# Kernel optimization log

Measured on AMD Instinct MI355X. Metric: run time of the kernel, lower is better.

Reference implementation:

```python
import jax, jax.numpy as jnp
import numpy as np

B, T, F_IN, D_PROJ, D_M, NH, DH, D_FF, OUT = 512, 100, 384, 128, 100, 4, 25, 400, 100
KS, SIGMA = 5, 1.0

def gaussian_kernel(size, sigma):
    c = jnp.arange(size, dtype=jnp.float32) - (size - 1) / 2.0
    x, y = jnp.meshgrid(c, c, indexing='ij')  # torch.meshgrid default is 'ij'
    k = jnp.exp(-(x ** 2 + y ** 2) / (2.0 * sigma ** 2))
    return k / k.sum()

def layer_norm(x, g, b, eps=1e-5):
    m = x.mean(-1, keepdims=True)
    v = ((x - m) ** 2).mean(-1, keepdims=True)
    return (x - m) / jnp.sqrt(v + eps) * g + b

def setup_inputs():
    key = jax.random.key(0)
    ks = jax.random.split(key, 20)
    la = jax.random.randint(ks[0], (B,), 2, T + 1)
    lc = jax.random.randint(ks[1], (B,), 2, T + 1)
    ar = jnp.arange(T)
    anchor_mask = (ar[None, :] < la[:, None]).astype(jnp.float32)
    comparison_mask = (ar[None, :] < lc[:, None]).astype(jnp.float32)
    p = lambda k, sh: jax.random.normal(k, sh, jnp.float32) * 0.02
    return dict(
        anco_speech=jax.random.normal(ks[2], (B, T, F_IN), jnp.float32),
        anchor_mask=anchor_mask,
        com_speech=jax.random.normal(ks[3], (B, T, F_IN), jnp.float32),
        comparison_mask=comparison_mask,
        anco_text=jax.random.normal(ks[4], (B, 128, 768), jnp.float32),
        label=jax.random.uniform(ks[5], (B,), jnp.float32),
        ln_an_g=jnp.ones(F_IN), ln_an_b=jnp.zeros(F_IN),
        W_an=p(ks[6], (F_IN, D_PROJ)), b_an=jnp.zeros(D_PROJ),
        ln_com_g=jnp.ones(F_IN), ln_com_b=jnp.zeros(F_IN),
        W_com=p(ks[7], (F_IN, D_PROJ)), b_com=jnp.zeros(D_PROJ),
        Wq=p(ks[8], (D_M, D_M)), bq=jnp.zeros(D_M),
        Wk=p(ks[9], (D_M, D_M)), bk=jnp.zeros(D_M),
        Wv=p(ks[10], (D_M, D_M)), bv=jnp.zeros(D_M),
        Wo=p(ks[11], (D_M, D_M)), bo=jnp.zeros(D_M),
        ln1_g=jnp.ones(D_M), ln1_b=jnp.zeros(D_M),
        Wff1=p(ks[12], (D_M, D_FF)), bff1=jnp.zeros(D_FF),
        Wff2=p(ks[13], (D_FF, D_M)), bff2=jnp.zeros(D_M),
        ln2_g=jnp.ones(D_M), ln2_b=jnp.zeros(D_M),
        W_ih=p(ks[14], (3 * OUT, D_M)), W_hh=p(ks[15], (3 * OUT, OUT)),
        b_ih=jnp.zeros(3 * OUT), b_hh=jnp.zeros(3 * OUT),
        W_fc=p(ks[16], (OUT, OUT)), b_fc=jnp.zeros(OUT),
        W_dense=p(ks[17], (OUT, 1)), b_dense=jnp.zeros(1))

def _bilinear_to_TxT(s, na, nc):
    # align_corners=True bilinear upsample of the valid [na, nc] top-left block of s to [T, T]
    t = jnp.arange(T, dtype=jnp.float32)
    sr = t * (na - 1).astype(jnp.float32) / (T - 1)
    sc = t * (nc - 1).astype(jnp.float32) / (T - 1)
    r0 = jnp.floor(sr).astype(jnp.int32); r1 = jnp.minimum(r0 + 1, na - 1); wr = sr - r0
    c0 = jnp.floor(sc).astype(jnp.int32); c1 = jnp.minimum(c0 + 1, nc - 1); wc = sc - c0
    v00 = s[r0[:, None], c0[None, :]]; v01 = s[r0[:, None], c1[None, :]]
    v10 = s[r1[:, None], c0[None, :]]; v11 = s[r1[:, None], c1[None, :]]
    top = v00 * (1 - wc)[None, :] + v01 * wc[None, :]
    bot = v10 * (1 - wc)[None, :] + v11 * wc[None, :]
    return top * (1 - wr)[:, None] + bot * wr[:, None]

def _forward(anco_speech, anchor_mask, com_speech, comparison_mask,
             ln_an_g, ln_an_b, W_an, b_an, ln_com_g, ln_com_b, W_com, b_com,
             Wq, bq, Wk, bk, Wv, bv, Wo, bo, ln1_g, ln1_b, Wff1, bff1, Wff2, bff2,
             ln2_g, ln2_b, W_ih, W_hh, b_ih, b_hh, W_fc, b_fc, W_dense, b_dense):
    # Projection adapters (LayerNorm -> Linear -> SiLU)
    an_p = jax.nn.silu(layer_norm(anco_speech, ln_an_g, ln_an_b) @ W_an + b_an)
    co_p = jax.nn.silu(layer_norm(com_speech, ln_com_g, ln_com_b) @ W_com + b_com)
    # masked cross cosine similarity [B, T, T]
    an_n = an_p / jnp.clip(jnp.linalg.norm(an_p, axis=-1, keepdims=True), 1e-8)
    co_n = co_p / jnp.clip(jnp.linalg.norm(co_p, axis=-1, keepdims=True), 1e-8)
    sim = jnp.einsum('bid,bjd->bij', an_n, co_n)
    sim = sim * anchor_mask[:, :, None] * comparison_mask[:, None, :]
    # ragged per-sample bilinear upsample of valid block to (100,100), vectorized via vmap
    la = anchor_mask.sum(1).astype(jnp.int32)
    lc = comparison_mask.sum(1).astype(jnp.int32)
    up = jax.vmap(_bilinear_to_TxT)(sim, la, lc)  # [B, T, T]
    # gaussian smoothing, kernel 5, padding 2 (== SAME)
    gk = gaussian_kernel(KS, SIGMA)[None, None]  # [1,1,5,5]
    sm = jax.lax.conv_general_dilated(up[:, None], gk, (1, 1), 'SAME',
                                      dimension_numbers=('NCHW', 'OIHW', 'NCHW'))[:, 0]
    # transformer encoder layer (post-norm, relu, 4 heads)
    q = (sm @ Wq + bq).reshape(B, T, NH, DH)
    k = (sm @ Wk + bk).reshape(B, T, NH, DH)
    v = (sm @ Wv + bv).reshape(B, T, NH, DH)
    att = jax.nn.softmax(jnp.einsum('bihd,bjhd->bhij', q, k) / np.float32(np.sqrt(DH)), axis=-1)
    ao = jnp.einsum('bhij,bjhd->bihd', att, v).reshape(B, T, D_M) @ Wo + bo
    x = layer_norm(sm + ao, ln1_g, ln1_b)
    x = layer_norm(x + jax.nn.relu(x @ Wff1 + bff1) @ Wff2 + bff2, ln2_g, ln2_b)
    # GRU over time, keep last hidden
    def step(h, xt):
        gi = xt @ W_ih.T + b_ih
        gh = h @ W_hh.T + b_hh
        ir, iz, inn = jnp.split(gi, 3, -1)
        hr, hz, hn = jnp.split(gh, 3, -1)
        r = jax.nn.sigmoid(ir + hr)
        z = jax.nn.sigmoid(iz + hz)
        n = jnp.tanh(inn + r * hn)
        return (1 - z) * n + z * h, None
    h0 = jnp.zeros((B, OUT), x.dtype)
    hT, _ = jax.lax.scan(step, h0, x.transpose(1, 0, 2))
    return (hT @ W_fc + b_fc) @ W_dense + b_dense  # [B, 1]

def reference(anco_speech, anchor_mask, com_speech, comparison_mask, anco_text, label,
              ln_an_g, ln_an_b, W_an, b_an, ln_com_g, ln_com_b, W_com, b_com,
              Wq, bq, Wk, bk, Wv, bv, Wo, bo, ln1_g, ln1_b, Wff1, bff1, Wff2, bff2,
              ln2_g, ln2_b, W_ih, W_hh, b_ih, b_hh, W_fc, b_fc, W_dense, b_dense):
    # anco_text and label are unused by the original forward
    return _forward(anco_speech, anchor_mask, com_speech, comparison_mask,
                    ln_an_g, ln_an_b, W_an, b_an, ln_com_g, ln_com_b, W_com, b_com,
                    Wq, bq, Wk, bk, Wv, bv, Wo, bo, ln1_g, ln1_b, Wff1, bff1, Wff2, bff2,
                    ln2_g, ln2_b, W_ih, W_hh, b_ih, b_hh, W_fc, b_fc, W_dense, b_dense)
```

## Files before the change

kernel.cpp:

```cpp
#include <hip/hip_runtime.h>
#include <cmath>

#define NB 512
#define NT 100
#define NROW (NB*NT)
#define FIN 384
#define DP 128

struct GW { float w[5]; };

__global__ __launch_bounds__(128) void k_lalc(const float* __restrict__ am, const float* __restrict__ cm,
                                              int* __restrict__ la, int* __restrict__ lc)
{
  __shared__ float s0[128], s1[128];
  int b = blockIdx.x, tid = threadIdx.x;
  s0[tid] = (tid < NT) ? am[b*NT+tid] : 0.0f;
  s1[tid] = (tid < NT) ? cm[b*NT+tid] : 0.0f;
  __syncthreads();
  for (int off = 64; off > 0; off >>= 1) {
    if (tid < off) { s0[tid] += s0[tid+off]; s1[tid] += s1[tid+off]; }
    __syncthreads();
  }
  if (tid == 0) { la[b] = (int)(s0[0] + 0.5f); lc[b] = (int)(s1[0] + 0.5f); }
}

__global__ __launch_bounds__(256) void k1_proj(
    const float* __restrict__ xin, const float* __restrict__ lng, const float* __restrict__ lnb,
    const float* __restrict__ W, const float* __restrict__ bias, float* __restrict__ out)
{
  const int tid = threadIdx.x;
  const int row0 = blockIdx.x * 32;
  __shared__ float xs[32*388];
  __shared__ float ps[256];
  __shared__ float ms[32];
  __shared__ float rs[32];
  __shared__ float inorm[32];

  const float4* x4 = (const float4*)(xin + (size_t)row0*FIN);
  for (int idx = tid; idx < 32*96; idx += 256) {
    int r = idx/96, k4 = idx%96;
    ((float4*)xs)[r*97 + k4] = x4[idx];
  }
  __syncthreads();
  {
    int r = tid>>3, p = tid&7;
    float s = 0; const float* xr = xs + r*388 + p*48;
    #pragma unroll
    for (int k=0;k<48;k++) s += xr[k];
    ps[tid] = s;
  }
  __syncthreads();
  if (tid < 32) { float s=0; for (int p=0;p<8;p++) s += ps[tid*8+p]; ms[tid] = s*(1.0f/FIN); }
  __syncthreads();
  {
    int r = tid>>3, p = tid&7;
    float m = ms[r], s=0; const float* xr = xs + r*388 + p*48;
    for (int k=0;k<48;k++){ float d = xr[k]-m; s += d*d; }
    ps[tid] = s;
  }
  __syncthreads();
  if (tid < 32) { float s=0; for (int p=0;p<8;p++) s += ps[tid*8+p]; rs[tid] = rsqrtf(s*(1.0f/FIN) + 1e-5f); }
  __syncthreads();
  for (int idx = tid; idx < 32*FIN; idx += 256) {
    int r = idx/FIN, k = idx%FIN;
    xs[r*388+k] = (xs[r*388+k]-ms[r])*rs[r]*lng[k] + lnb[k];
  }
  __syncthreads();
  const int jg = tid & 31, rg = tid >> 5;
  float acc[4][4] = {};
  const float4* W4 = (const float4*)W;
  for (int k = 0; k < FIN; k++) {
    float4 wv = W4[k*32 + jg];
    #pragma unroll
    for (int rr = 0; rr < 4; rr++) {
      float xv = xs[(rg*4+rr)*388 + k];
      acc[rr][0] += xv*wv.x; acc[rr][1] += xv*wv.y;
      acc[rr][2] += xv*wv.z; acc[rr][3] += xv*wv.w;
    }
  }
  __syncthreads();
  #pragma unroll
  for (int rr = 0; rr < 4; rr++) {
    int r = rg*4+rr;
    #pragma unroll
    for (int c = 0; c < 4; c++) {
      float pv = acc[rr][c] + bias[jg*4+c];
      xs[r*132 + jg*4 + c] = pv * (1.0f/(1.0f+__expf(-pv)));
    }
  }
  __syncthreads();
  {
    int r = tid>>3, p = tid&7;
    float s = 0; const float* xr = xs + r*132 + p*16;
    #pragma unroll
    for (int k=0;k<16;k++) s += xr[k]*xr[k];
    ps[tid] = s;
  }
  __syncthreads();
  if (tid < 32) { float s=0; for (int p=0;p<8;p++) s += ps[tid*8+p]; inorm[tid] = 1.0f/fmaxf(sqrtf(s), 1e-8f); }
  __syncthreads();
  float4* o4 = (float4*)(out + (size_t)row0*DP);
  for (int idx = tid; idx < 32*32; idx += 256) {
    int r = idx/32, k4 = idx%32;
    float4 v = ((float4*)xs)[r*33 + k4];
    float s = inorm[r];
    v.x*=s; v.y*=s; v.z*=s; v.w*=s;
    o4[idx] = v;
  }
}

__global__ __launch_bounds__(256) void k2_sim(const float* __restrict__ An, const float* __restrict__ Co,
                                              float* __restrict__ S)
{
  int b = blockIdx.x, tid = threadIdx.x;
  __shared__ float as_[100*132];
  __shared__ float bs_[100*132];
  const float4* A4 = (const float4*)(An + (size_t)b*NT*DP);
  const float4* B4 = (const float4*)(Co + (size_t)b*NT*DP);
  for (int idx = tid; idx < 100*32; idx += 256) {
    int r = idx>>5, k4 = idx&31;
    ((float4*)as_)[r*33+k4] = A4[idx];
    ((float4*)bs_)[r*33+k4] = B4[idx];
  }
  __syncthreads();
  int ti = tid>>4, tj = tid&15;
  float acc[7][7] = {};
  for (int k4 = 0; k4 < 32; k4++) {
    float4 av[7], bv[7];
    #pragma unroll
    for (int m=0;m<7;m++){ int i = ti+16*m; if (i>99) i=99; av[m] = ((float4*)as_)[i*33+k4]; }
    #pragma unroll
    for (int n=0;n<7;n++){ int j = tj+16*n; if (j>99) j=99; bv[n] = ((float4*)bs_)[j*33+k4]; }
    #pragma unroll
    for (int m=0;m<7;m++)
      #pragma unroll
      for (int n=0;n<7;n++)
        acc[m][n] += av[m].x*bv[n].x + av[m].y*bv[n].y + av[m].z*bv[n].z + av[m].w*bv[n].w;
  }
  float* Sb = S + (size_t)b*NT*NT;
  #pragma unroll
  for (int m=0;m<7;m++){ int i = ti+16*m; if (i>99) continue;
    #pragma unroll
    for (int n=0;n<7;n++){ int j = tj+16*n; if (j>99) continue;
      Sb[i*100+j] = acc[m][n];
    } }
}

__global__ __launch_bounds__(256) void k3_bilinear(const float* __restrict__ S, float* __restrict__ U,
                                                   const int* __restrict__ la, const int* __restrict__ lc)
{
  int b = blockIdx.x, tid = threadIdx.x;
  int na = la[b], nc = lc[b];
  const float* Sb = S + (size_t)b*10000;
  float* Ub = U + (size_t)b*10000;
  for (int idx = tid; idx < 10000; idx += 256) {
    int i = idx/100, j = idx%100;
    float sr = (float)(i*(na-1)) / 99.0f;
    float sc = (float)(j*(nc-1)) / 99.0f;
    int r0 = (int)sr, c0 = (int)sc;
    float wr = sr - (float)r0, wc = sc - (float)c0;
    int r1 = r0+1; if (r1 > na-1) r1 = na-1;
    int c1 = c0+1; if (c1 > nc-1) c1 = nc-1;
    float v00 = Sb[r0*100+c0], v01 = Sb[r0*100+c1];
    float v10 = Sb[r1*100+c0], v11 = Sb[r1*100+c1];
    float top = v00*(1.0f-wc) + v01*wc;
    float bot = v10*(1.0f-wc) + v11*wc;
    Ub[idx] = top*(1.0f-wr) + bot*wr;
  }
}

__global__ __launch_bounds__(256) void k4_conv(const float* __restrict__ U, float* __restrict__ S, GW gw)
{
  int b = blockIdx.x, tid = threadIdx.x;
  __shared__ float us[100*104];
  __shared__ float ts[100*104];
  const float4* U4 = (const float4*)(U + (size_t)b*10000);
  for (int idx = tid; idx < 100*25; idx += 256) {
    int r = idx/25, k4 = idx%25;
    ((float4*)us)[r*26+k4] = U4[idx];
  }
  __syncthreads();
  for (int idx = tid; idx < 10000; idx += 256) {
    int i = idx/100, j = idx%100;
    float s = 0;
    #pragma unroll
    for (int d = -2; d <= 2; d++) {
      int jj = j + d;
      if (jj >= 0 && jj < 100) s += gw.w[d+2] * us[i*104+jj];
    }
    ts[i*104+j] = s;
  }
  __syncthreads();
  float* Sb = S + (size_t)b*10000;
  for (int idx = tid; idx < 10000; idx += 256) {
    int i = idx/100, j = idx%100;
    float s = 0;
    #pragma unroll
    for (int d = -2; d <= 2; d++) {
      int ii = i + d;
      if (ii >= 0 && ii < 100) s += gw.w[d+2] * ts[ii*104+j];
    }
    Sb[idx] = s;
  }
}

__global__ __launch_bounds__(256) void k5_qkv(const float* __restrict__ SM,
    const float* __restrict__ Wq, const float* __restrict__ bq,
    const float* __restrict__ Wk, const float* __restrict__ bk,
    const float* __restrict__ Wv, const float* __restrict__ bv,
    float* __restrict__ Q, float* __restrict__ K, float* __restrict__ V)
{
  int tid = threadIdx.x;
  int row0 = blockIdx.x * 32;
  __shared__ float xs[32*104];
  const float4* X4 = (const float4*)(SM + (size_t)row0*100);
  for (int idx = tid; idx < 32*25; idx += 256) {
    int r = idx/25, k4 = idx%25;
    ((float4*)xs)[r*26+k4] = X4[idx];
  }
  __syncthreads();
  int jg = tid&31, rg = tid>>5;
  for (int jt = 0; jt < 3; jt++) {
    int j0 = jt*128 + jg*4;
    if (j0 < 300) {
      const float* Wsel; const float* bsel; float* Osel; int jj;
      if (j0 < 100)      { Wsel=Wq; bsel=bq; Osel=Q; jj=j0; }
      else if (j0 < 200) { Wsel=Wk; bsel=bk; Osel=K; jj=j0-100; }
      else               { Wsel=Wv; bsel=bv; Osel=V; jj=j0-200; }
      float acc[4][4] = {};
      const float4* W4 = (const float4*)Wsel;
      for (int k = 0; k < 100; k++) {
        float4 wv = W4[k*25 + (jj>>2)];
        #pragma unroll
        for (int rr=0; rr<4; rr++) {
          float xv = xs[(rg*4+rr)*104 + k];
          acc[rr][0]+=xv*wv.x; acc[rr][1]+=xv*wv.y; acc[rr][2]+=xv*wv.z; acc[rr][3]+=xv*wv.w;
        }
      }
      float4 bv4 = ((const float4*)bsel)[jj>>2];
      #pragma unroll
      for (int rr=0; rr<4; rr++) {
        int r = row0 + rg*4 + rr;
        float4 o; o.x=acc[rr][0]+bv4.x; o.y=acc[rr][1]+bv4.y; o.z=acc[rr][2]+bv4.z; o.w=acc[rr][3]+bv4.w;
        *(float4*)(Osel + (size_t)r*100 + jj) = o;
      }
    }
  }
}

__global__ __launch_bounds__(256) void k6_attn(const float* __restrict__ Q, const float* __restrict__ K,
                                               const float* __restrict__ V, float* __restrict__ HO)
{
  int b = blockIdx.x, h = blockIdx.y, tid = threadIdx.x;
  __shared__ float qs[100*28], ks[100*28], vs[100*28];
  __shared__ float ss[100*101];
  for (int idx = tid; idx < 2500; idx += 256) {
    int r = idx/25, d = idx%25;
    size_t g = (size_t)(b*100+r)*100 + h*25 + d;
    qs[r*28+d] = Q[g]; ks[r*28+d] = K[g]; vs[r*28+d] = V[g];
  }
  __syncthreads();
  int ti = tid>>4, tj = tid&15;
  {
    float acc[7][7] = {};
    for (int d4 = 0; d4 < 6; d4++) {
      float4 qv[7], kv[7];
      #pragma unroll
      for (int m=0;m<7;m++){ int i=ti+16*m; if(i>99)i=99; qv[m]=((float4*)qs)[i*7+d4]; }
      #pragma unroll
      for (int n=0;n<7;n++){ int j=tj+16*n; if(j>99)j=99; kv[n]=((float4*)ks)[j*7+d4]; }
      #pragma unroll
      for (int m=0;m<7;m++)
        #pragma unroll
        for (int n=0;n<7;n++)
          acc[m][n] += qv[m].x*kv[n].x + qv[m].y*kv[n].y + qv[m].z*kv[n].z + qv[m].w*kv[n].w;
    }
    {
      float qv[7], kv[7];
      #pragma unroll
      for (int m=0;m<7;m++){ int i=ti+16*m; if(i>99)i=99; qv[m]=qs[i*28+24]; }
      #pragma unroll
      for (int n=0;n<7;n++){ int j=tj+16*n; if(j>99)j=99; kv[n]=ks[j*28+24]; }
      #pragma unroll
      for (int m=0;m<7;m++)
        #pragma unroll
        for (int n=0;n<7;n++) acc[m][n] += qv[m]*kv[n];
    }
    #pragma unroll
    for (int m=0;m<7;m++){ int i=ti+16*m; if (i>99) continue;
      #pragma unroll
      for (int n=0;n<7;n++){ int j=tj+16*n; if (j>99) continue;
        ss[i*101+j] = acc[m][n]*(1.0f/5.0f);
      } }
  }
  __syncthreads();
  if (tid < 100) {
    float* row = ss + tid*101;
    float mx = -1e30f;
    for (int j=0;j<100;j++) mx = fmaxf(mx, row[j]);
    float sum = 0;
    for (int j=0;j<100;j++){ float e = __expf(row[j]-mx); row[j] = e; sum += e; }
    float inv = 1.0f/sum;
    for (int j=0;j<100;j++) row[j] *= inv;
  }
  __syncthreads();
  {
    int d0 = tj;
    float acc0[7] = {}, acc1[7] = {};
    for (int j = 0; j < 100; j++) {
      float v0 = vs[j*28 + d0];
      float v1 = (tj < 9) ? vs[j*28 + d0 + 16] : 0.0f;
      #pragma unroll
      for (int m=0;m<7;m++) {
        int i = ti+16*m; if (i>99) i = 99;
        float p = ss[i*101+j];
        acc0[m] += p*v0; acc1[m] += p*v1;
      }
    }
    #pragma unroll
    for (int m=0;m<7;m++) {
      int i = ti+16*m; if (i>99) continue;
      size_t g = (size_t)(b*100+i)*100 + h*25;
      HO[g + d0] = acc0[m];
      if (tj < 9) HO[g + d0 + 16] = acc1[m];
    }
  }
}

__device__ __forceinline__ void row_ln_100(float* ybuf, float* ps, float* ms, float* rs,
                                           const float* g, const float* bta, int tid)
{
  {
    int r = tid>>3, p = tid&7;
    int kb = p*13, ke = kb+13; if (ke>100) ke=100;
    float s=0; const float* yr = ybuf + r*104;
    for (int k=kb;k<ke;k++) s += yr[k];
    ps[tid]=s;
  }
  __syncthreads();
  if (tid<32){ float s=0; for(int p=0;p<8;p++) s+=ps[tid*8+p]; ms[tid]=s*(1.0f/100.0f); }
  __syncthreads();
  {
    int r = tid>>3, p = tid&7;
    int kb = p*13, ke = kb+13; if (ke>100) ke=100;
    float m = ms[r], s=0; const float* yr = ybuf + r*104;
    for (int k=kb;k<ke;k++){ float d=yr[k]-m; s+=d*d; }
    ps[tid]=s;
  }
  __syncthreads();
  if (tid<32){ float s=0; for(int p=0;p<8;p++) s+=ps[tid*8+p]; rs[tid]=rsqrtf(s*(1.0f/100.0f)+1e-5f); }
  __syncthreads();
  for (int idx=tid; idx<3200; idx+=256){
    int r = idx/100, k = idx%100;
    ybuf[r*104+k] = (ybuf[r*104+k]-ms[r])*rs[r]*g[k] + bta[k];
  }
  __syncthreads();
}

__global__ __launch_bounds__(256) void k7_ln1(const float* __restrict__ HOin, const float* __restrict__ Wo,
    const float* __restrict__ bo, const float* __restrict__ SM,
    const float* __restrict__ g1, const float* __restrict__ b1v, float* __restrict__ X)
{
  int tid = threadIdx.x;
  int row0 = blockIdx.x * 32;
  __shared__ float hsd[32*104];
  __shared__ float ys[32*104];
  __shared__ float ps[256];
  __shared__ float ms[32], rs[32];
  const float4* H4 = (const float4*)(HOin + (size_t)row0*100);
  for (int idx = tid; idx < 32*25; idx += 256) {
    int r = idx/25, k4 = idx%25;
    ((float4*)hsd)[r*26+k4] = H4[idx];
  }
  __syncthreads();
  int jg = tid&31, rg = tid>>5;
  if (jg < 25) {
    int j0 = jg*4;
    float acc[4][4] = {};
    const float4* W4 = (const float4*)Wo;
    for (int k=0;k<100;k++) {
      float4 wv = W4[k*25 + jg];
      #pragma unroll
      for (int rr=0;rr<4;rr++){
        float xv = hsd[(rg*4+rr)*104+k];
        acc[rr][0]+=xv*wv.x; acc[rr][1]+=xv*wv.y; acc[rr][2]+=xv*wv.z; acc[rr][3]+=xv*wv.w;
      }
    }
    float4 bv = ((const float4*)bo)[jg];
    #pragma unroll
    for (int rr=0;rr<4;rr++){
      int r = rg*4+rr;
      float4 smv = ((const float4*)(SM + (size_t)(row0+r)*100))[jg];
      float4 o; o.x = acc[rr][0]+bv.x+smv.x; o.y = acc[rr][1]+bv.y+smv.y;
      o.z = acc[rr][2]+bv.z+smv.z; o.w = acc[rr][3]+bv.w+smv.w;
      *(float4*)&ys[r*104 + j0] = o;
    }
  }
  __syncthreads();
  row_ln_100(ys, ps, ms, rs, g1, b1v, tid);
  float4* X4o = (float4*)(X + (size_t)row0*100);
  for (int idx=tid; idx<32*25; idx+=256){
    int r = idx/25, k4 = idx%25;
    X4o[idx] = ((float4*)ys)[r*26+k4];
  }
}

__global__ __launch_bounds__(256) void k8_ffn(const float* __restrict__ X,
    const float* __restrict__ W1, const float* __restrict__ b1f,
    const float* __restrict__ W2, const float* __restrict__ b2f,
    const float* __restrict__ g2, const float* __restrict__ bt2, float* __restrict__ X2)
{
  int tid = threadIdx.x;
  int row0 = blockIdx.x * 32;
  __shared__ float xs[32*104];
  __shared__ float hh[32*404];
  __shared__ float ps[256];
  __shared__ float ms[32], rs[32];
  const float4* X4 = (const float4*)(X + (size_t)row0*100);
  for (int idx = tid; idx < 32*25; idx += 256) {
    int r=idx/25,k4=idx%25; ((float4*)xs)[r*26+k4] = X4[idx];
  }
  __syncthreads();
  int jg = tid&31, rg = tid>>5;
  const float4* W14 = (const float4*)W1;
  for (int jt = 0; jt < 4; jt++) {
    int j0 = jt*128 + jg*4;
    if (j0 < 400) {
      float acc[4][4] = {};
      for (int k=0;k<100;k++){
        float4 wv = W14[k*100 + (j0>>2)];
        #pragma unroll
        for (int rr=0;rr<4;rr++){
          float xv = xs[(rg*4+rr)*104+k];
          acc[rr][0]+=xv*wv.x; acc[rr][1]+=xv*wv.y; acc[rr][2]+=xv*wv.z; acc[rr][3]+=xv*wv.w;
        }
      }
      float4 bv = ((const float4*)b1f)[j0>>2];
      #pragma unroll
      for (int rr=0;rr<4;rr++){
        int r = rg*4+rr;
        float4 o;
        o.x=fmaxf(acc[rr][0]+bv.x,0.0f); o.y=fmaxf(acc[rr][1]+bv.y,0.0f);
        o.z=fmaxf(acc[rr][2]+bv.z,0.0f); o.w=fmaxf(acc[rr][3]+bv.w,0.0f);
        *(float4*)&hh[r*404 + j0] = o;
      }
    }
  }
  __syncthreads();
  float4 yv[4];
  if (jg < 25) {
    int j0 = jg*4;
    float acc[4][4] = {};
    const float4* W24 = (const float4*)W2;
    for (int k=0;k<400;k++){
      float4 wv = W24[k*25 + jg];
      #pragma unroll
      for (int rr=0;rr<4;rr++){
        float xv = hh[(rg*4+rr)*404+k];
        acc[rr][0]+=xv*wv.x; acc[rr][1]+=xv*wv.y; acc[rr][2]+=xv*wv.z; acc[rr][3]+=xv*wv.w;
      }
    }
    float4 bv = ((const float4*)b2f)[jg];
    #pragma unroll
    for (int rr=0;rr<4;rr++){
      int r=rg*4+rr;
      yv[rr].x=acc[rr][0]+bv.x+xs[r*104+j0+0];
      yv[rr].y=acc[rr][1]+bv.y+xs[r*104+j0+1];
      yv[rr].z=acc[rr][2]+bv.z+xs[r*104+j0+2];
      yv[rr].w=acc[rr][3]+bv.w+xs[r*104+j0+3];
    }
  }
  __syncthreads();
  if (jg < 25) {
    int j0 = jg*4;
    #pragma unroll
    for (int rr=0;rr<4;rr++) *(float4*)&xs[(rg*4+rr)*104+j0] = yv[rr];
  }
  __syncthreads();
  row_ln_100(xs, ps, ms, rs, g2, bt2, tid);
  float4* O4 = (float4*)(X2 + (size_t)row0*100);
  for (int idx=tid; idx<32*25; idx+=256){
    int r=idx/25,k4=idx%25; O4[idx] = ((float4*)xs)[r*26+k4];
  }
}

__global__ void k_tr(const float* __restrict__ A, float* __restrict__ AT)
{
  int idx = blockIdx.x*256 + threadIdx.x;
  if (idx < 300*100){ int g = idx/100, k = idx%100; AT[k*300+g] = A[idx]; }
}

__global__ __launch_bounds__(256) void k9_gi(const float* __restrict__ X2, const float* __restrict__ WT,
    const float* __restrict__ bih, float* __restrict__ GIv)
{
  int tid = threadIdx.x;
  int row0 = blockIdx.x * 32;
  __shared__ float xs[32*104];
  const float4* X4 = (const float4*)(X2 + (size_t)row0*100);
  for (int idx = tid; idx < 32*25; idx += 256){ int r=idx/25,k4=idx%25; ((float4*)xs)[r*26+k4]=X4[idx]; }
  __syncthreads();
  int jg = tid&31, rg = tid>>5;
  const float4* W4 = (const float4*)WT;
  for (int jt=0; jt<3; jt++){
    int j0 = jt*128 + jg*4;
    if (j0 < 300) {
      float acc[4][4] = {};
      for (int k=0;k<100;k++){
        float4 wv = W4[k*75 + (j0>>2)];
        #pragma unroll
        for (int rr=0;rr<4;rr++){
          float xv = xs[(rg*4+rr)*104+k];
          acc[rr][0]+=xv*wv.x; acc[rr][1]+=xv*wv.y; acc[rr][2]+=xv*wv.z; acc[rr][3]+=xv*wv.w;
        }
      }
      float4 bv = ((const float4*)bih)[j0>>2];
      #pragma unroll
      for (int rr=0;rr<4;rr++){
        int r = row0 + rg*4+rr;
        int bb = r/100, t = r%100;
        float4 o; o.x=acc[rr][0]+bv.x; o.y=acc[rr][1]+bv.y; o.z=acc[rr][2]+bv.z; o.w=acc[rr][3]+bv.w;
        *(float4*)(GIv + ((size_t)t*512 + bb)*300 + j0) = o;
      }
    }
  }
}

__global__ __launch_bounds__(320) void k10_gru(const float* __restrict__ GIv, const float* __restrict__ Whh,
    const float* __restrict__ bhh, float* __restrict__ HT)
{
  int tid = threadIdx.x;
  int r0 = blockIdx.x*2;
  __shared__ float4 W4[7500];
  __shared__ float hs[2][100];
  __shared__ float ghs[2][300];
  __shared__ float gis[2][300];
  __shared__ float bhs[300];
  const float4* Wg4 = (const float4*)Whh;
  for (int idx = tid; idx < 7500; idx += 320) {
    int g = idx/25, k4 = idx%25;
    W4[k4*300+g] = Wg4[g*25+k4];
  }
  if (tid < 300) bhs[tid] = bhh[tid];
  if (tid < 200) hs[tid/100][tid%100] = 0.0f;
  __syncthreads();
  for (int t = 0; t < 100; t++) {
    if (tid < 300) {
      gis[0][tid] = GIv[((size_t)t*512 + r0)*300 + tid];
      gis[1][tid] = GIv[((size_t)t*512 + r0+1)*300 + tid];
      float a0 = 0, a1 = 0;
      const float4* h40 = (const float4*)hs[0];
      const float4* h41 = (const float4*)hs[1];
      #pragma unroll
      for (int k4 = 0; k4 < 25; k4++) {
        float4 w = W4[k4*300 + tid];
        float4 h0 = h40[k4];
        float4 h1 = h41[k4];
        a0 += w.x*h0.x + w.y*h0.y + w.z*h0.z + w.w*h0.w;
        a1 += w.x*h1.x + w.y*h1.y + w.z*h1.z + w.w*h1.w;
      }
      float bb = bhs[tid];
      ghs[0][tid] = a0 + bb;
      ghs[1][tid] = a1 + bb;
    }
    __syncthreads();
    if (tid < 200) {
      int rr = tid/100, j = tid%100;
      float rg = 1.0f/(1.0f+__expf(-(gis[rr][j]     + ghs[rr][j])));
      float zg = 1.0f/(1.0f+__expf(-(gis[rr][j+100] + ghs[rr][j+100])));
      float ng = tanhf(gis[rr][j+200] + rg*ghs[rr][j+200]);
      float hold = hs[rr][j];
      hs[rr][j] = (1.0f-zg)*ng + zg*hold;
    }
    __syncthreads();
  }
  if (tid < 200) HT[(size_t)(r0 + tid/100)*100 + tid%100] = hs[tid/100][tid%100];
}

__global__ __launch_bounds__(128) void k_out(const float* __restrict__ HT, const float* __restrict__ Wfc,
    const float* __restrict__ bfc, const float* __restrict__ Wd, const float* __restrict__ bd,
    float* __restrict__ out)
{
  __shared__ float red[128];
  int b = blockIdx.x, tid = threadIdx.x;
  float s = 0;
  if (tid < 100) {
    float v = 0;
    for (int j = 0; j < 100; j++) v += Wfc[tid*100+j]*Wd[j];
    s = HT[(size_t)b*100+tid]*v + bfc[tid]*Wd[tid];
  }
  red[tid] = s;
  __syncthreads();
  for (int off = 64; off > 0; off >>= 1) {
    if (tid < off) red[tid] += red[tid+off];
    __syncthreads();
  }
  if (tid == 0) out[b] = red[0] + bd[0];
}

extern "C" void kernel_launch(void* const* d_in, const int* in_sizes, int n_in,
                              void* d_out, int out_size, void* d_ws, size_t ws_size,
                              hipStream_t stream)
{
  const float* anco  = (const float*)d_in[0];
  const float* amask = (const float*)d_in[1];
  const float* comsp = (const float*)d_in[2];
  const float* cmask = (const float*)d_in[3];
  const float* ln_an_g = (const float*)d_in[6];
  const float* ln_an_b = (const float*)d_in[7];
  const float* W_an  = (const float*)d_in[8];
  const float* b_an  = (const float*)d_in[9];
  const float* ln_co_g = (const float*)d_in[10];
  const float* ln_co_b = (const float*)d_in[11];
  const float* W_co  = (const float*)d_in[12];
  const float* b_co  = (const float*)d_in[13];
  const float* Wq = (const float*)d_in[14]; const float* bq = (const float*)d_in[15];
  const float* Wk = (const float*)d_in[16]; const float* bk = (const float*)d_in[17];
  const float* Wv = (const float*)d_in[18]; const float* bv = (const float*)d_in[19];
  const float* Wo = (const float*)d_in[20]; const float* bo = (const float*)d_in[21];
  const float* ln1g = (const float*)d_in[22]; const float* ln1b = (const float*)d_in[23];
  const float* W1 = (const float*)d_in[24]; const float* b1 = (const float*)d_in[25];
  const float* W2 = (const float*)d_in[26]; const float* b2 = (const float*)d_in[27];
  const float* ln2g = (const float*)d_in[28]; const float* ln2b = (const float*)d_in[29];
  const float* Wih = (const float*)d_in[30]; const float* Whh = (const float*)d_in[31];
  const float* bih = (const float*)d_in[32]; const float* bhh = (const float*)d_in[33];
  const float* Wfc = (const float*)d_in[34]; const float* bfc = (const float*)d_in[35];
  const float* Wd  = (const float*)d_in[36]; const float* bd  = (const float*)d_in[37];

  float* ws = (float*)d_ws;
  float* AN = ws;
  float* CO = ws + 6553600;
  float* S  = ws + 13107200;
  float* U  = ws + 18227200;
  float* Dh = ws + 23347200;
  float* GIp = ws + 13107200;
  float* HT = ws + 28467200;
  float* WT = ws + 28518400;
  int* la = (int*)(ws + 28548500);
  int* lc = la + 512;

  GW gw;
  {
    float e[5], sum = 0;
    for (int i=0;i<5;i++){ float c = (float)i - 2.0f; e[i] = expf(-(c*c)/2.0f); sum += e[i]; }
    for (int i=0;i<5;i++) gw.w[i] = e[i]/sum;
  }

  k_lalc<<<512,128,0,stream>>>(amask, cmask, la, lc);
  k1_proj<<<1600,256,0,stream>>>(anco,  ln_an_g, ln_an_b, W_an, b_an, AN);
  k1_proj<<<1600,256,0,stream>>>(comsp, ln_co_g, ln_co_b, W_co, b_co, CO);
  k2_sim<<<512,256,0,stream>>>(AN, CO, S);
  k3_bilinear<<<512,256,0,stream>>>(S, U, la, lc);
  k4_conv<<<512,256,0,stream>>>(U, S, gw);
  k5_qkv<<<1600,256,0,stream>>>(S, Wq,bq, Wk,bk, Wv,bv, AN, CO, U);
  k6_attn<<<dim3(512,4),256,0,stream>>>(AN, CO, U, Dh);
  k7_ln1<<<1600,256,0,stream>>>(Dh, Wo, bo, S, ln1g, ln1b, AN);
  k8_ffn<<<1600,256,0,stream>>>(AN, W1,b1, W2,b2, ln2g, ln2b, CO);
  k_tr<<<118,256,0,stream>>>(Wih, WT);
  k9_gi<<<1600,256,0,stream>>>(CO, WT, bih, GIp);
  k10_gru<<<256,320,0,stream>>>(GIp, Whh, bhh, HT);
  k_out<<<512,128,0,stream>>>(HT, Wfc, bfc, Wd, bd, (float*)d_out);
}
```

Measured before the change: 1.461 ms.

## Port projection, QKV, FFN and GRU-input GEMMs to bf16 MFMA

Adds a prep kernel that transposes and pads the weights into bf16. The input projection, QKV, FFN and GRU input-gate matmuls now run on bf16 16x16x32 MFMA instructions instead of scalar fp32 FMA loops. The FFN's LayerNorm is redone with wave shuffles, and its output is stored as padded bf16 that feeds k9 directly, which also removes the separate Wih transpose kernel. Rounding activations and weights to bf16 lowers precision, and there is one extra prep launch per call.

```diff
diff --git a/kernel.cpp b/kernel.cpp
--- a/kernel.cpp
+++ b/kernel.cpp
@@ -9,6 +9,44 @@
 
 struct GW { float w[5]; };
 
+typedef __attribute__((ext_vector_type(8))) short bf16x8;
+typedef __attribute__((ext_vector_type(4))) float f32x4;
+
+__device__ __forceinline__ unsigned short f2bf(float f){
+  union { float f; unsigned u; } v; v.f = f;
+  unsigned u = v.u;
+  return (unsigned short)((u + 0x7FFFu + ((u>>16)&1u)) >> 16);
+}
+__device__ __forceinline__ float bf2f(unsigned short h){
+  union { unsigned u; float f; } v; v.u = ((unsigned)h)<<16; return v.f;
+}
+
+__global__ __launch_bounds__(256) void k_prep(const float* __restrict__ Wan, const float* __restrict__ Wco,
+    const float* __restrict__ Wq, const float* __restrict__ Wk, const float* __restrict__ Wv,
+    const float* __restrict__ bq, const float* __restrict__ bk, const float* __restrict__ bv,
+    const float* __restrict__ W1, const float* __restrict__ W2, const float* __restrict__ Wih,
+    unsigned short* __restrict__ WanT, unsigned short* __restrict__ WcoT,
+    unsigned short* __restrict__ WqkvT, unsigned short* __restrict__ W1T,
+    unsigned short* __restrict__ W2T, unsigned short* __restrict__ WihT,
+    float* __restrict__ bqkv)
+{
+  int idx = blockIdx.x*256 + threadIdx.x;
+  if (idx < 49152) { int j = idx/384, k = idx%384; WanT[idx] = f2bf(Wan[k*128+j]); }
+  else if (idx < 98304) { int i = idx-49152; int j = i/384, k = i%384; WcoT[i] = f2bf(Wco[k*128+j]); }
+  else if (idx < 137216) { int i = idx-98304; int j = i/128, k = i%128;
+    float v = 0.0f;
+    if (k < 100 && j < 300) v = (j < 100) ? Wq[k*100+j] : ((j < 200) ? Wk[k*100+j-100] : Wv[k*100+j-200]);
+    WqkvT[i] = f2bf(v); }
+  else if (idx < 188416) { int i = idx-137216; int j = i/128, k = i%128;
+    W1T[i] = f2bf(k < 100 ? W1[k*400+j] : 0.0f); }
+  else if (idx < 238592) { int i = idx-188416; int j = i/448, k = i%448;
+    W2T[i] = f2bf((j < 100 && k < 400) ? W2[k*100+j] : 0.0f); }
+  else if (idx < 277504) { int i = idx-238592; int j = i/128, k = i%128;
+    WihT[i] = f2bf((k < 100 && j < 300) ? Wih[j*100+k] : 0.0f); }
+  else if (idx < 277804) { int j = idx-277504;
+    bqkv[j] = (j < 100) ? bq[j] : ((j < 200) ? bk[j-100] : bv[j-200]); }
+}
+
 __global__ __launch_bounds__(128) void k_lalc(const float* __restrict__ am, const float* __restrict__ cm,
                                               int* __restrict__ la, int* __restrict__ lc)
 {
@@ -26,25 +64,24 @@
 
 __global__ __launch_bounds__(256) void k1_proj(
     const float* __restrict__ xin, const float* __restrict__ lng, const float* __restrict__ lnb,
-    const float* __restrict__ W, const float* __restrict__ bias, float* __restrict__ out)
+    const unsigned short* __restrict__ WT, const float* __restrict__ bias, float* __restrict__ out)
 {
   const int tid = threadIdx.x;
   const int row0 = blockIdx.x * 32;
-  __shared__ float xs[32*388];
+  __shared__ float xf[32*388];
   __shared__ float ps[256];
-  __shared__ float ms[32];
-  __shared__ float rs[32];
-  __shared__ float inorm[32];
+  __shared__ float ms[32], rs[32], inorm[32];
+  float* ys = xf;
 
   const float4* x4 = (const float4*)(xin + (size_t)row0*FIN);
   for (int idx = tid; idx < 32*96; idx += 256) {
     int r = idx/96, k4 = idx%96;
-    ((float4*)xs)[r*97 + k4] = x4[idx];
+    ((float4*)xf)[r*97 + k4] = x4[idx];
   }
   __syncthreads();
   {
     int r = tid>>3, p = tid&7;
-    float s = 0; const float* xr = xs + r*388 + p*48;
+    float s = 0; const float* xr = xf + r*388 + p*48;
     #pragma unroll
     for (int k=0;k<48;k++) s += xr[k];
     ps[tid] = s;
@@ -54,7 +91,7 @@
   __syncthreads();
   {
     int r = tid>>3, p = tid&7;
-    float m = ms[r], s=0; const float* xr = xs + r*388 + p*48;
+    float m = ms[r], s=0; const float* xr = xf + r*388 + p*48;
     for (int k=0;k<48;k++){ float d = xr[k]-m; s += d*d; }
     ps[tid] = s;
   }
@@ -63,35 +100,49 @@
   __syncthreads();
   for (int idx = tid; idx < 32*FIN; idx += 256) {
     int r = idx/FIN, k = idx%FIN;
-    xs[r*388+k] = (xs[r*388+k]-ms[r])*rs[r]*lng[k] + lnb[k];
-  }
-  __syncthreads();
-  const int jg = tid & 31, rg = tid >> 5;
-  float acc[4][4] = {};
-  const float4* W4 = (const float4*)W;
-  for (int k = 0; k < FIN; k++) {
-    float4 wv = W4[k*32 + jg];
-    #pragma unroll
-    for (int rr = 0; rr < 4; rr++) {
-      float xv = xs[(rg*4+rr)*388 + k];
-      acc[rr][0] += xv*wv.x; acc[rr][1] += xv*wv.y;
-      acc[rr][2] += xv*wv.z; acc[rr][3] += xv*wv.w;
-    }
-  }
-  __syncthreads();
-  #pragma unroll
-  for (int rr = 0; rr < 4; rr++) {
-    int r = rg*4+rr;
-    #pragma unroll
-    for (int c = 0; c < 4; c++) {
-      float pv = acc[rr][c] + bias[jg*4+c];
-      xs[r*132 + jg*4 + c] = pv * (1.0f/(1.0f+__expf(-pv)));
+    xf[r*388+k] = (xf[r*388+k]-ms[r])*rs[r]*lng[k] + lnb[k];
+  }
+  __syncthreads();
+  const int l = tid & 63, w = tid >> 6;
+  const int lh = l & 15, lq = l >> 4;
+  const int rt = w & 1, nh = w >> 1;
+  bf16x8 afr[12];
+  {
+    const int row = rt*16 + lh;
+    const float* xr = &xf[row*388 + lq*8];
+    #pragma unroll
+    for (int kb = 0; kb < 12; kb++) {
+      float4 u0 = *(const float4*)(xr + kb*32);
+      float4 u1 = *(const float4*)(xr + kb*32 + 4);
+      bf16x8 a;
+      a[0]=(short)f2bf(u0.x); a[1]=(short)f2bf(u0.y); a[2]=(short)f2bf(u0.z); a[3]=(short)f2bf(u0.w);
+      a[4]=(short)f2bf(u1.x); a[5]=(short)f2bf(u1.y); a[6]=(short)f2bf(u1.z); a[7]=(short)f2bf(u1.w);
+      afr[kb] = a;
+    }
+  }
+  __syncthreads();
+  for (int nt2 = 0; nt2 < 4; nt2++) {
+    int nt = nh*4 + nt2;
+    int j = nt*16 + lh;
+    f32x4 acc = {0.f,0.f,0.f,0.f};
+    const unsigned short* wp = &WT[(size_t)j*384 + lq*8];
+    #pragma unroll
+    for (int kb = 0; kb < 12; kb++) {
+      bf16x8 b = *(const bf16x8*)(wp + kb*32);
+      acc = __builtin_amdgcn_mfma_f32_16x16x32_bf16(afr[kb], b, acc, 0, 0, 0);
+    }
+    float bj = bias[j];
+    #pragma unroll
+    for (int p = 0; p < 4; p++) {
+      float v = acc[p] + bj;
+      v = v * (1.0f/(1.0f+__expf(-v)));
+      ys[(rt*16 + lq*4 + p)*132 + j] = v;
     }
   }
   __syncthreads();
   {
     int r = tid>>3, p = tid&7;
-    float s = 0; const float* xr = xs + r*132 + p*16;
+    float s = 0; const float* xr = ys + r*132 + p*16;
     #pragma unroll
     for (int k=0;k<16;k++) s += xr[k]*xr[k];
     ps[tid] = s;
@@ -102,7 +153,7 @@
   float4* o4 = (float4*)(out + (size_t)row0*DP);
   for (int idx = tid; idx < 32*32; idx += 256) {
     int r = idx/32, k4 = idx%32;
-    float4 v = ((float4*)xs)[r*33 + k4];
+    float4 v = ((float4*)ys)[r*33 + k4];
     float s = inorm[r];
     v.x*=s; v.y*=s; v.z*=s; v.w*=s;
     o4[idx] = v;
@@ -205,45 +256,51 @@
 }
 
 __global__ __launch_bounds__(256) void k5_qkv(const float* __restrict__ SM,
-    const float* __restrict__ Wq, const float* __restrict__ bq,
-    const float* __restrict__ Wk, const float* __restrict__ bk,
-    const float* __restrict__ Wv, const float* __restrict__ bv,
+    const unsigned short* __restrict__ WT, const float* __restrict__ bqkv,
     float* __restrict__ Q, float* __restrict__ K, float* __restrict__ V)
 {
-  int tid = threadIdx.x;
-  int row0 = blockIdx.x * 32;
-  __shared__ float xs[32*104];
+  const int tid = threadIdx.x;
+  const int row0 = blockIdx.x * 64;
+  __shared__ unsigned short xsb[64*128];
   const float4* X4 = (const float4*)(SM + (size_t)row0*100);
-  for (int idx = tid; idx < 32*25; idx += 256) {
+  for (int idx = tid; idx < 64*25; idx += 256) {
     int r = idx/25, k4 = idx%25;
-    ((float4*)xs)[r*26+k4] = X4[idx];
-  }
-  __syncthreads();
-  int jg = tid&31, rg = tid>>5;
-  for (int jt = 0; jt < 3; jt++) {
-    int j0 = jt*128 + jg*4;
-    if (j0 < 300) {
-      const float* Wsel; const float* bsel; float* Osel; int jj;
-      if (j0 < 100)      { Wsel=Wq; bsel=bq; Osel=Q; jj=j0; }
-      else if (j0 < 200) { Wsel=Wk; bsel=bk; Osel=K; jj=j0-100; }
-      else               { Wsel=Wv; bsel=bv; Osel=V; jj=j0-200; }
-      float acc[4][4] = {};
-      const float4* W4 = (const float4*)Wsel;
-      for (int k = 0; k < 100; k++) {
-        float4 wv = W4[k*25 + (jj>>2)];
-        #pragma unroll
-        for (int rr=0; rr<4; rr++) {
-          float xv = xs[(rg*4+rr)*104 + k];
-          acc[rr][0]+=xv*wv.x; acc[rr][1]+=xv*wv.y; acc[rr][2]+=xv*wv.z; acc[rr][3]+=xv*wv.w;
-        }
-      }
-      float4 bv4 = ((const float4*)bsel)[jj>>2];
-      #pragma unroll
-      for (int rr=0; rr<4; rr++) {
-        int r = row0 + rg*4 + rr;
-        float4 o; o.x=acc[rr][0]+bv4.x; o.y=acc[rr][1]+bv4.y; o.z=acc[rr][2]+bv4.z; o.w=acc[rr][3]+bv4.w;
-        *(float4*)(Osel + (size_t)r*100 + jj) = o;
-      }
+    float4 v = X4[idx];
+    ushort4 pk = make_ushort4(f2bf(v.x), f2bf(v.y), f2bf(v.z), f2bf(v.w));
+    *(ushort4*)&xsb[r*128 + ((k4*4) ^ ((r&7)<<3))] = pk;
+  }
+  for (int idx = tid; idx < 64*28; idx += 256) {
+    int r = idx/28, k = 100 + idx%28;
+    xsb[r*128 + (k ^ ((r&7)<<3))] = 0;
+  }
+  __syncthreads();
+  const int l = tid & 63, w = tid >> 6;
+  const int lh = l & 15, lq = l >> 4;
+  const int arow = w*16 + lh;
+  bf16x8 afr[4];
+  #pragma unroll
+  for (int kb = 0; kb < 4; kb++)
+    afr[kb] = *(const bf16x8*)&xsb[arow*128 + ((kb*32 + lq*8) ^ ((arow&7)<<3))];
+  int orow[4];
+  #pragma unroll
+  for (int p=0;p<4;p++) orow[p] = row0 + w*16 + lq*4 + p;
+  for (int nt = 0; nt < 19; nt++) {
+    int j = nt*16 + lh;
+    f32x4 acc = {0.f,0.f,0.f,0.f};
+    const unsigned short* wp = &WT[(size_t)j*128 + lq*8];
+    #pragma unroll
+    for (int kb = 0; kb < 4; kb++) {
+      bf16x8 b = *(const bf16x8*)(wp + kb*32);
+      acc = __builtin_amdgcn_mfma_f32_16x16x32_bf16(afr[kb], b, acc, 0, 0, 0);
+    }
+    if (j < 300) {
+      float bj = bqkv[j];
+      float* dst; int col;
+      if (j < 100)      { dst = Q; col = j; }
+      else if (j < 200) { dst = K; col = j-100; }
+      else              { dst = V; col = j-200; }
+      #pragma unroll
+      for (int p=0;p<4;p++) dst[(size_t)orow[p]*100 + col] = acc[p] + bj;
     }
   }
 }
@@ -406,121 +463,156 @@
 }
 
 __global__ __launch_bounds__(256) void k8_ffn(const float* __restrict__ X,
-    const float* __restrict__ W1, const float* __restrict__ b1f,
-    const float* __restrict__ W2, const float* __restrict__ b2f,
-    const float* __restrict__ g2, const float* __restrict__ bt2, float* __restrict__ X2)
-{
-  int tid = threadIdx.x;
-  int row0 = blockIdx.x * 32;
-  __shared__ float xs[32*104];
-  __shared__ float hh[32*404];
-  __shared__ float ps[256];
-  __shared__ float ms[32], rs[32];
+    const unsigned short* __restrict__ W1T, const float* __restrict__ b1f,
+    const unsigned short* __restrict__ W2T, const float* __restrict__ b2f,
+    const float* __restrict__ g2, const float* __restrict__ bt2,
+    unsigned short* __restrict__ X2bf)
+{
+  const int tid = threadIdx.x;
+  const int row0 = blockIdx.x * 64;
+  __shared__ unsigned short xsb[64*128];
+  __shared__ unsigned short hh[64*448];
   const float4* X4 = (const float4*)(X + (size_t)row0*100);
-  for (int idx = tid; idx < 32*25; idx += 256) {
-    int r=idx/25,k4=idx%25; ((float4*)xs)[r*26+k4] = X4[idx];
-  }
-  __syncthreads();
-  int jg = tid&31, rg = tid>>5;
-  const float4* W14 = (const float4*)W1;
-  for (int jt = 0; jt < 4; jt++) {
-    int j0 = jt*128 + jg*4;
-    if (j0 < 400) {
-      float acc[4][4] = {};
-      for (int k=0;k<100;k++){
-        float4 wv = W14[k*100 + (j0>>2)];
-        #pragma unroll
-        for (int rr=0;rr<4;rr++){
-          float xv = xs[(rg*4+rr)*104+k];
-          acc[rr][0]+=xv*wv.x; acc[rr][1]+=xv*wv.y; acc[rr][2]+=xv*wv.z; acc[rr][3]+=xv*wv.w;
-        }
-      }
-      float4 bv = ((const float4*)b1f)[j0>>2];
-      #pragma unroll
-      for (int rr=0;rr<4;rr++){
-        int r = rg*4+rr;
-        float4 o;
-        o.x=fmaxf(acc[rr][0]+bv.x,0.0f); o.y=fmaxf(acc[rr][1]+bv.y,0.0f);
-        o.z=fmaxf(acc[rr][2]+bv.z,0.0f); o.w=fmaxf(acc[rr][3]+bv.w,0.0f);
-        *(float4*)&hh[r*404 + j0] = o;
-      }
-    }
-  }
-  __syncthreads();
-  float4 yv[4];
-  if (jg < 25) {
-    int j0 = jg*4;
-    float acc[4][4] = {};
-    const float4* W24 = (const float4*)W2;
-    for (int k=0;k<400;k++){
-      float4 wv = W24[k*25 + jg];
-      #pragma unroll
-      for (int rr=0;rr<4;rr++){
-        float xv = hh[(rg*4+rr)*404+k];
-        acc[rr][0]+=xv*wv.x; acc[rr][1]+=xv*wv.y; acc[rr][2]+=xv*wv.z; acc[rr][3]+=xv*wv.w;
-      }
-    }
-    float4 bv = ((const float4*)b2f)[jg];
-    #pragma unroll
-    for (int rr=0;rr<4;rr++){
-      int r=rg*4+rr;
-      yv[rr].x=acc[rr][0]+bv.x+xs[r*104+j0+0];
-      yv[rr].y=acc[rr][1]+bv.y+xs[r*104+j0+1];
-      yv[rr].z=acc[rr][2]+bv.z+xs[r*104+j0+2];
-      yv[rr].w=acc[rr][3]+bv.w+xs[r*104+j0+3];
-    }
-  }
-  __syncthreads();
-  if (jg < 25) {
-    int j0 = jg*4;
-    #pragma unroll
-    for (int rr=0;rr<4;rr++) *(float4*)&xs[(rg*4+rr)*104+j0] = yv[rr];
-  }
-  __syncthreads();
-  row_ln_100(xs, ps, ms, rs, g2, bt2, tid);
-  float4* O4 = (float4*)(X2 + (size_t)row0*100);
-  for (int idx=tid; idx<32*25; idx+=256){
-    int r=idx/25,k4=idx%25; O4[idx] = ((float4*)xs)[r*26+k4];
-  }
-}
-
-__global__ void k_tr(const float* __restrict__ A, float* __restrict__ AT)
-{
-  int idx = blockIdx.x*256 + threadIdx.x;
-  if (idx < 300*100){ int g = idx/100, k = idx%100; AT[k*300+g] = A[idx]; }
-}
-
-__global__ __launch_bounds__(256) void k9_gi(const float* __restrict__ X2, const float* __restrict__ WT,
-    const float* __restrict__ bih, float* __restrict__ GIv)
-{
-  int tid = threadIdx.x;
-  int row0 = blockIdx.x * 32;
-  __shared__ float xs[32*104];
-  const float4* X4 = (const float4*)(X2 + (size_t)row0*100);
-  for (int idx = tid; idx < 32*25; idx += 256){ int r=idx/25,k4=idx%25; ((float4*)xs)[r*26+k4]=X4[idx]; }
-  __syncthreads();
-  int jg = tid&31, rg = tid>>5;
-  const float4* W4 = (const float4*)WT;
-  for (int jt=0; jt<3; jt++){
-    int j0 = jt*128 + jg*4;
-    if (j0 < 300) {
-      float acc[4][4] = {};
-      for (int k=0;k<100;k++){
-        float4 wv = W4[k*75 + (j0>>2)];
-        #pragma unroll
-        for (int rr=0;rr<4;rr++){
-          float xv = xs[(rg*4+rr)*104+k];
-          acc[rr][0]+=xv*wv.x; acc[rr][1]+=xv*wv.y; acc[rr][2]+=xv*wv.z; acc[rr][3]+=xv*wv.w;
-        }
-      }
-      float4 bv = ((const float4*)bih)[j0>>2];
-      #pragma unroll
-      for (int rr=0;rr<4;rr++){
-        int r = row0 + rg*4+rr;
-        int bb = r/100, t = r%100;
-        float4 o; o.x=acc[rr][0]+bv.x; o.y=acc[rr][1]+bv.y; o.z=acc[rr][2]+bv.z; o.w=acc[rr][3]+bv.w;
-        *(float4*)(GIv + ((size_t)t*512 + bb)*300 + j0) = o;
-      }
+  for (int idx = tid; idx < 64*25; idx += 256) {
+    int r = idx/25, k4 = idx%25;
+    float4 v = X4[idx];
+    ushort4 pk = make_ushort4(f2bf(v.x), f2bf(v.y), f2bf(v.z), f2bf(v.w));
+    *(ushort4*)&xsb[r*128 + ((k4*4) ^ ((r&7)<<3))] = pk;
+  }
+  for (int idx = tid; idx < 64*28; idx += 256) {
+    int r = idx/28, k = 100 + idx%28;
+    xsb[r*128 + (k ^ ((r&7)<<3))] = 0;
+  }
+  __syncthreads();
+  const int l = tid & 63, w = tid >> 6;
+  const int lh = l & 15, lq = l >> 4;
+  const int arow = w*16 + lh;
+  bf16x8 a1[4];
+  #pragma unroll
+  for (int kb=0;kb<4;kb++)
+    a1[kb] = *(const bf16x8*)&xsb[arow*128 + ((kb*32+lq*8) ^ ((arow&7)<<3))];
+  int drow[4];
+  #pragma unroll
+  for (int p=0;p<4;p++) drow[p] = w*16 + lq*4 + p;
+  for (int nt = 0; nt < 25; nt++) {
+    int j = nt*16 + lh;
+    f32x4 acc = {0.f,0.f,0.f,0.f};
+    const unsigned short* wp = &W1T[(size_t)j*128 + lq*8];
+    #pragma unroll
+    for (int kb=0;kb<4;kb++) {
+      bf16x8 b = *(const bf16x8*)(wp + kb*32);
+      acc = __builtin_amdgcn_mfma_f32_16x16x32_bf16(a1[kb], b, acc, 0, 0, 0);
+    }
+    float bj = b1f[j];
+    #pragma unroll
+    for (int p=0;p<4;p++) {
+      float hv = fmaxf(acc[p] + bj, 0.0f);
+      hh[drow[p]*448 + (j ^ ((drow[p]&7)<<3))] = f2bf(hv);
+    }
+  }
+  for (int i = l; i < 16*48; i += 64) {
+    int r = w*16 + i/48, c = 400 + i%48;
+    hh[r*448 + (c ^ ((r&7)<<3))] = 0;
+  }
+  bf16x8 a2[13];
+  #pragma unroll
+  for (int kb=0;kb<13;kb++)
+    a2[kb] = *(const bf16x8*)&hh[arow*448 + ((kb*32+lq*8) ^ ((arow&7)<<3))];
+  __syncthreads();
+  unsigned short* ob = hh;
+  float y[7][4];
+  #pragma unroll
+  for (int nt=0; nt<7; nt++) {
+    int j = nt*16 + lh;
+    f32x4 acc = {0.f,0.f,0.f,0.f};
+    const unsigned short* wp = &W2T[(size_t)j*448 + lq*8];
+    #pragma unroll
+    for (int kb=0;kb<13;kb++) {
+      bf16x8 b = *(const bf16x8*)(wp + kb*32);
+      acc = __builtin_amdgcn_mfma_f32_16x16x32_bf16(a2[kb], b, acc, 0, 0, 0);
+    }
+    bool valid = (j < 100);
+    float bj = valid ? b2f[j] : 0.0f;
+    #pragma unroll
+    for (int p=0;p<4;p++) {
+      float resid = valid ? bf2f(xsb[drow[p]*128 + (j ^ ((drow[p]&7)<<3))]) : 0.0f;
+      y[nt][p] = valid ? (acc[p] + bj + resid) : 0.0f;
+    }
+  }
+  float mm[4], ri[4];
+  #pragma unroll
+  for (int p=0;p<4;p++) {
+    float s = 0;
+    #pragma unroll
+    for (int nt=0;nt<7;nt++) s += y[nt][p];
+    s += __shfl_xor(s,1); s += __shfl_xor(s,2); s += __shfl_xor(s,4); s += __shfl_xor(s,8);
+    mm[p] = s * 0.01f;
+    float v = 0;
+    #pragma unroll
+    for (int nt=0;nt<7;nt++) {
+      int j = nt*16+lh;
+      if (j < 100) { float d = y[nt][p]-mm[p]; v += d*d; }
+    }
+    v += __shfl_xor(v,1); v += __shfl_xor(v,2); v += __shfl_xor(v,4); v += __shfl_xor(v,8);
+    ri[p] = rsqrtf(v*0.01f + 1e-5f);
+  }
+  #pragma unroll
+  for (int nt=0;nt<7;nt++) {
+    int j = nt*16+lh;
+    float gj = (j<100) ? g2[j] : 0.0f;
+    float bj = (j<100) ? bt2[j] : 0.0f;
+    #pragma unroll
+    for (int p=0;p<4;p++) {
+      unsigned short o = 0;
+      if (j < 100) o = f2bf((y[nt][p]-mm[p])*ri[p]*gj + bj);
+      ob[drow[p]*128 + (j ^ ((drow[p]&7)<<3))] = o;
+    }
+  }
+  #pragma unroll
+  for (int p=0;p<4;p++) {
+    int c = 112 + lh;
+    ob[drow[p]*128 + (c ^ ((drow[p]&7)<<3))] = 0;
+  }
+  __syncthreads();
+  ushort4* dst4 = (ushort4*)(X2bf + (size_t)row0*128);
+  for (int idx = tid; idx < 64*32; idx += 256) {
+    int r = idx/32, c4 = idx%32;
+    dst4[idx] = *(const ushort4*)&ob[r*128 + ((c4*4) ^ ((r&7)<<3))];
+  }
+}
+
+__global__ __launch_bounds__(256) void k9_gi(const unsigned short* __restrict__ X2bf,
+    const unsigned short* __restrict__ WihT, const float* __restrict__ bih, float* __restrict__ GIv)
+{
+  const int tid = threadIdx.x;
+  const int row0 = blockIdx.x * 64;
+  const int l = tid & 63, w = tid >> 6;
+  const int lh = l & 15, lq = l >> 4;
+  const int row = row0 + w*16 + lh;
+  bf16x8 afr[4];
+  #pragma unroll
+  for (int kb=0;kb<4;kb++)
+    afr[kb] = *(const bf16x8*)&X2bf[(size_t)row*128 + kb*32 + lq*8];
+  size_t obase[4];
+  #pragma unroll
+  for (int p=0;p<4;p++) {
+    int gr = row0 + w*16 + lq*4 + p;
+    int bb = gr/100, t = gr%100;
+    obase[p] = ((size_t)t*512 + bb)*300;
+  }
+  for (int nt=0; nt<19; nt++) {
+    int j = nt*16 + lh;
+    f32x4 acc = {0.f,0.f,0.f,0.f};
+    const unsigned short* wp = &WihT[(size_t)j*128 + lq*8];
+    #pragma unroll
+    for (int kb=0;kb<4;kb++) {
+      bf16x8 b = *(const bf16x8*)(wp + kb*32);
+      acc = __builtin_amdgcn_mfma_f32_16x16x32_bf16(afr[kb], b, acc, 0, 0, 0);
+    }
+    if (j < 300) {
+      float bj = bih[j];
+      #pragma unroll
+      for (int p=0;p<4;p++) GIv[obase[p] + j] = acc[p] + bj;
     }
   }
 }
@@ -634,9 +726,17 @@
   float* Dh = ws + 23347200;
   float* GIp = ws + 13107200;
   float* HT = ws + 28467200;
-  float* WT = ws + 28518400;
-  int* la = (int*)(ws + 28548500);
+  int* la = (int*)(ws + 28518400);
   int* lc = la + 512;
+  unsigned short* X2bf = (unsigned short*)CO;
+  unsigned short* WB = (unsigned short*)(ws + 28520000);
+  unsigned short* WanT  = WB;
+  unsigned short* WcoT  = WB + 49152;
+  unsigned short* WqkvT = WB + 98304;
+  unsigned short* W1T   = WB + 137216;
+  unsigned short* W2T   = WB + 188416;
+  unsigned short* WihT  = WB + 238592;
+  float* bqkv = ws + 28660000;
 
   GW gw;
   {
@@ -645,18 +745,19 @@
     for (int i=0;i<5;i++) gw.w[i] = e[i]/sum;
   }
 
+  k_prep<<<1086,256,0,stream>>>(W_an, W_co, Wq, Wk, Wv, bq, bk, bv, W1, W2, Wih,
+                                WanT, WcoT, WqkvT, W1T, W2T, WihT, bqkv);
   k_lalc<<<512,128,0,stream>>>(amask, cmask, la, lc);
-  k1_proj<<<1600,256,0,stream>>>(anco,  ln_an_g, ln_an_b, W_an, b_an, AN);
-  k1_proj<<<1600,256,0,stream>>>(comsp, ln_co_g, ln_co_b, W_co, b_co, CO);
+  k1_proj<<<1600,256,0,stream>>>(anco,  ln_an_g, ln_an_b, WanT, b_an, AN);
+  k1_proj<<<1600,256,0,stream>>>(comsp, ln_co_g, ln_co_b, WcoT, b_co, CO);
   k2_sim<<<512,256,0,stream>>>(AN, CO, S);
   k3_bilinear<<<512,256,0,stream>>>(S, U, la, lc);
   k4_conv<<<512,256,0,stream>>>(U, S, gw);
-  k5_qkv<<<1600,256,0,stream>>>(S, Wq,bq, Wk,bk, Wv,bv, AN, CO, U);
+  k5_qkv<<<800,256,0,stream>>>(S, WqkvT, bqkv, AN, CO, U);
   k6_attn<<<dim3(512,4),256,0,stream>>>(AN, CO, U, Dh);
   k7_ln1<<<1600,256,0,stream>>>(Dh, Wo, bo, S, ln1g, ln1b, AN);
-  k8_ffn<<<1600,256,0,stream>>>(AN, W1,b1, W2,b2, ln2g, ln2b, CO);
-  k_tr<<<118,256,0,stream>>>(Wih, WT);
-  k9_gi<<<1600,256,0,stream>>>(CO, WT, bih, GIp);
+  k8_ffn<<<800,256,0,stream>>>(AN, W1T, b1, W2T, b2, ln2g, ln2b, X2bf);
+  k9_gi<<<800,256,0,stream>>>(X2bf, WihT, bih, GIp);
   k10_gru<<<256,320,0,stream>>>(GIp, Whh, bhh, HT);
   k_out<<<512,128,0,stream>>>(HT, Wfc, bfc, Wd, bd, (float*)d_out);
 }
```

After: 1.197 ms. 1.22x faster.
